# Performance work log

Measured on AMD Instinct MI355X. Metric: run time of the kernel, lower is better.

## Reference

```python
import jax, jax.numpy as jnp
import numpy as np

GAMMA = 2.0

def _bce_with_logits(x, y):
    # stable: max(x,0) - x*y + log(1+exp(-|x|)) == logaddexp(0,x) - x*y
    return jnp.logaddexp(0.0, x) - x * y

def setup_inputs() -> dict:
    key = jax.random.key(0)
    k1, k2, k3 = jax.random.split(key, 3)
    B = 4_000_000
    logit = jax.random.normal(k1, (B, 7), dtype=jnp.float32)
    label = jax.random.randint(k2, (B,), 0, 2, dtype=jnp.int32)
    repr_mask = jax.random.randint(k3, (B, 7), 0, 2, dtype=jnp.int32)
    return {"logit": logit, "label": label, "repr_mask": repr_mask}

def reference(logit, label, repr_mask):
    B = logit.shape[0]
    logit = logit.reshape(B, -1)                     # [B,7]
    lab = label.astype(logit.dtype)[:, None]         # [B,1], broadcasts like repeat(1,7)
    bce = _bce_with_logits(logit, lab)               # [B,7]
    focal = (1.0 - jnp.exp(-bce)) ** GAMMA * bce
    bce_neg = _bce_with_logits(-logit, 1.0 - lab)
    focal_neg = (1.0 - jnp.exp(-bce_neg)) ** GAMMA * bce_neg
    m = repr_mask.astype(logit.dtype)                # 1 on repr indices
    pos = jnp.sum(focal * m, axis=1)                 # sum over repr_num[i]
    neg = jnp.sum(focal_neg * (1.0 - m), axis=1)     # sum over not_repr
    is_neg_label = (label == 0)
    loss = pos + jnp.where(is_neg_label, neg, jnp.zeros_like(neg))
    return loss
```

## Files before the change

kernel.cpp:

```cpp
#include <hip/hip_runtime.h>


#define TPB 256
#define F4PB (TPB * 7)

__device__ __forceinline__ float focal_elem(float x, bool y1) {
    float e  = __expf(-fabsf(x));
    float r  = 1.0f / (1.0f + e);
    float q  = e * r;
    bool xpos = (x >= 0.0f);
    float pt = (y1 == xpos) ? r : q;
    float bce = -__logf(pt);
    float om  = 1.0f - pt;
    return om * om * bce;
}

__global__ __launch_bounds__(TPB) void focal_loss_kernel(
    const float* __restrict__ logit,
    const int*   __restrict__ label,
    const int*   __restrict__ repr_mask,
    float*       __restrict__ out,
    int B)
{
    __shared__ uint4 lds[F4PB];

    const int Q   = B >> 2;
    const int tid = threadIdx.x;
    const int q0  = blockIdx.x * TPB;
    const int nq  = min(TPB, Q - q0);
    const int nf4 = nq * 7;
    const bool active = tid < nq;

    const uint4* lg4 = reinterpret_cast<const uint4*>(logit)     + (size_t)q0 * 7;
    const uint4* mk4 = reinterpret_cast<const uint4*>(repr_mask) + (size_t)q0 * 7;

    int4 lab4 = make_int4(0, 0, 0, 0);
    if (active) lab4 = reinterpret_cast<const int4*>(label)[q0 + tid];

#pragma unroll
    for (int k = 0; k < 7; ++k) {
        int idx = tid + k * TPB;
        if (idx < nf4) lds[idx] = lg4[idx];
    }
    __syncthreads();

    bool y1[4] = { lab4.x != 0, lab4.y != 0, lab4.z != 0, lab4.w != 0 };
    float f[28];
    if (active) {
#pragma unroll
        for (int j = 0; j < 7; ++j) {
            uint4 u = lds[tid * 7 + j];
            float4 a = *reinterpret_cast<float4*>(&u);
            f[4*j+0] = a.x; f[4*j+1] = a.y; f[4*j+2] = a.z; f[4*j+3] = a.w;
        }
#pragma unroll
        for (int i = 0; i < 28; ++i)
            f[i] = focal_elem(f[i], y1[i / 7]);
    }
    __syncthreads();

#pragma unroll
    for (int k = 0; k < 7; ++k) {
        int idx = tid + k * TPB;
        if (idx < nf4) lds[idx] = mk4[idx];
    }
    __syncthreads();

    if (active) {
        float res[4] = {0.f, 0.f, 0.f, 0.f};
#pragma unroll
        for (int j = 0; j < 7; ++j) {
            uint4 m = lds[tid * 7 + j];
            unsigned mm[4] = { m.x, m.y, m.z, m.w };
#pragma unroll
            for (int k = 0; k < 4; ++k) {
                int i = 4*j + k;
                int r = i / 7;
                bool keep = y1[r] ? (mm[k] != 0) : true;
                res[r] += keep ? f[i] : 0.0f;
            }
        }
        reinterpret_cast<float4*>(out)[q0 + tid] =
            make_float4(res[0], res[1], res[2], res[3]);
    }

    if ((B & 3) && blockIdx.x == 0 && tid == 0) {
        for (int row = Q * 4; row < B; ++row) {
            bool yy = (label[row] != 0);
            float tot = 0.f, ms = 0.f;
            for (int c = 0; c < 7; ++c) {
                float ff = focal_elem(logit[(size_t)row * 7 + c], yy);
                tot += ff;
                ms  += repr_mask[(size_t)row * 7 + c] ? ff : 0.f;
            }
            out[row] = yy ? ms : tot;
        }
    }
}

extern "C" void kernel_launch(void* const* d_in, const int* in_sizes, int n_in,
                              void* d_out, int out_size, void* d_ws, size_t ws_size,
                              hipStream_t stream) {
    const float* logit     = (const float*)d_in[0];
    const int*   label     = (const int*)d_in[1];
    const int*   repr_mask = (const int*)d_in[2];
    float*       out       = (float*)d_out;

    int B = in_sizes[1];
    int Q = B >> 2;
    int blocks = (Q + TPB - 1) / TPB;
    if (blocks < 1) blocks = 1;

    focal_loss_kernel<<<blocks, TPB, 0, stream>>>(logit, label, repr_mask, out, B);
}
```

Baseline: 46.84 us.

## Use per-wave async global-to-LDS loads and overlap mask loads with logit staging

Each block now splits into independent per-wave LDS slices, so the block-wide __syncthreads barriers are gone. Logits go through global_load_lds directly into LDS, while mask loads are issued at the same time into registers and written to LDS after the logits are consumed. This removes the serial load-sync-compute-load-sync sequence, and launch bounds ask for 5 blocks per CU. It relies on an explicit vmcnt wait and on intra-wave ordering for LDS reuse, and it adds a scalar fallback path for partial waves.

```diff
diff --git a/kernel.cpp b/kernel.cpp
--- a/kernel.cpp
+++ b/kernel.cpp
@@ -1,8 +1,14 @@
 #include <hip/hip_runtime.h>
+#include <stdint.h>
 
 
 #define TPB 256
-#define F4PB (TPB * 7)
+#define U4W 448
+
+#define GLOAD_LDS16(gp, lp)                                         \
+    __builtin_amdgcn_global_load_lds(                               \
+        (const __attribute__((address_space(1))) void*)(gp),        \
+        (__attribute__((address_space(3))) void*)(lp), 16, 0, 0)
 
 __device__ __forceinline__ float focal_elem(float x, bool y1) {
     float e  = __expf(-fabsf(x));
@@ -15,62 +21,60 @@
     return om * om * bce;
 }
 
-__global__ __launch_bounds__(TPB) void focal_loss_kernel(
+__global__ __launch_bounds__(TPB, 5) void focal_loss_kernel(
     const float* __restrict__ logit,
     const int*   __restrict__ label,
     const int*   __restrict__ repr_mask,
     float*       __restrict__ out,
     int B)
 {
-    __shared__ uint4 lds[F4PB];
+    __shared__ uint4 lds[4][U4W];
 
-    const int Q   = B >> 2;
-    const int tid = threadIdx.x;
-    const int q0  = blockIdx.x * TPB;
-    const int nq  = min(TPB, Q - q0);
-    const int nf4 = nq * 7;
-    const bool active = tid < nq;
+    const int Q    = B >> 2;
+    const int tid  = threadIdx.x;
+    const int lane = tid & 63;
+    const int w    = tid >> 6;
+    const int q0   = blockIdx.x * TPB + w * 64;
 
-    const uint4* lg4 = reinterpret_cast<const uint4*>(logit)     + (size_t)q0 * 7;
-    const uint4* mk4 = reinterpret_cast<const uint4*>(repr_mask) + (size_t)q0 * 7;
+    uint4* wbuf = lds[w];
 
-    int4 lab4 = make_int4(0, 0, 0, 0);
-    if (active) lab4 = reinterpret_cast<const int4*>(label)[q0 + tid];
+    if (q0 + 64 <= Q) {
+        const uint4* lg4 = reinterpret_cast<const uint4*>(logit)     + (size_t)q0 * 7;
+        const uint4* mk4 = reinterpret_cast<const uint4*>(repr_mask) + (size_t)q0 * 7;
 
 #pragma unroll
-    for (int k = 0; k < 7; ++k) {
-        int idx = tid + k * TPB;
-        if (idx < nf4) lds[idx] = lg4[idx];
-    }
-    __syncthreads();
+        for (int k = 0; k < 7; ++k)
+            GLOAD_LDS16(lg4 + k * 64 + lane, wbuf + k * 64);
 
-    bool y1[4] = { lab4.x != 0, lab4.y != 0, lab4.z != 0, lab4.w != 0 };
-    float f[28];
-    if (active) {
+        int4 lab4 = reinterpret_cast<const int4*>(label)[q0 + lane];
+        uint4 mreg[7];
+#pragma unroll
+        for (int k = 0; k < 7; ++k)
+            mreg[k] = mk4[k * 64 + lane];
+
+        asm volatile("s_waitcnt vmcnt(0)" ::: "memory");
+
+        float f[28];
 #pragma unroll
         for (int j = 0; j < 7; ++j) {
-            uint4 u = lds[tid * 7 + j];
+            uint4 u = wbuf[lane * 7 + j];
             float4 a = *reinterpret_cast<float4*>(&u);
             f[4*j+0] = a.x; f[4*j+1] = a.y; f[4*j+2] = a.z; f[4*j+3] = a.w;
         }
+
+#pragma unroll
+        for (int k = 0; k < 7; ++k)
+            wbuf[k * 64 + lane] = mreg[k];
+
+        bool y1[4] = { lab4.x != 0, lab4.y != 0, lab4.z != 0, lab4.w != 0 };
 #pragma unroll
         for (int i = 0; i < 28; ++i)
             f[i] = focal_elem(f[i], y1[i / 7]);
-    }
-    __syncthreads();
 
-#pragma unroll
-    for (int k = 0; k < 7; ++k) {
-        int idx = tid + k * TPB;
-        if (idx < nf4) lds[idx] = mk4[idx];
-    }
-    __syncthreads();
-
-    if (active) {
         float res[4] = {0.f, 0.f, 0.f, 0.f};
 #pragma unroll
         for (int j = 0; j < 7; ++j) {
-            uint4 m = lds[tid * 7 + j];
+            uint4 m = wbuf[lane * 7 + j];
             unsigned mm[4] = { m.x, m.y, m.z, m.w };
 #pragma unroll
             for (int k = 0; k < 4; ++k) {
@@ -80,8 +84,29 @@
                 res[r] += keep ? f[i] : 0.0f;
             }
         }
-        reinterpret_cast<float4*>(out)[q0 + tid] =
+        reinterpret_cast<float4*>(out)[q0 + lane] =
             make_float4(res[0], res[1], res[2], res[3]);
+    } else if (q0 < Q) {
+        int r4 = q0 + lane;
+        if (r4 < Q) {
+            int lab = label[r4 * 4];
+            (void)lab;
+            float res[4];
+#pragma unroll
+            for (int r = 0; r < 4; ++r) {
+                int row = r4 * 4 + r;
+                bool yy = (label[row] != 0);
+                float tot = 0.f, ms = 0.f;
+                for (int c = 0; c < 7; ++c) {
+                    float ff = focal_elem(logit[(size_t)row * 7 + c], yy);
+                    tot += ff;
+                    ms  += repr_mask[(size_t)row * 7 + c] ? ff : 0.f;
+                }
+                res[r] = yy ? ms : tot;
+            }
+            reinterpret_cast<float4*>(out)[r4] =
+                make_float4(res[0], res[1], res[2], res[3]);
+        }
     }
 
     if ((B & 3) && blockIdx.x == 0 && tid == 0) {
```

Result: no change. 46.42 us (-0.9%).
